# Kernel tuning notes

Hardware: AMD Instinct MI355X
Metric: run time of the kernel (lower is better)

## Reference

```python
import jax, jax.numpy as jnp
import numpy as np

LN_EPS = 1e-5
DIM = 8        # pooled spatial size per axis -> token feature = DIM*DIM = 64
DIM_HEAD = 64


def setup_inputs() -> dict:
    key = jax.random.key(0)
    k1, k2, k3 = jax.random.split(key, 3)
    b, t, c, h, w = 8, 16, 64, 56, 56
    x = jax.random.normal(k1, (b, t, c, h, w), dtype=jnp.float32)
    pos_embedding = jax.random.normal(k2, (b * c, t, DIM * DIM), dtype=jnp.float32)
    # nn.Linear(dim*dim, 2*dim_head, bias=False); stored here as (in, out)
    W_qk = jax.random.normal(k3, (DIM * DIM, 2 * DIM_HEAD), dtype=jnp.float32) * (DIM * DIM) ** -0.5
    gamma = jnp.ones((DIM * DIM,), dtype=jnp.float32)
    beta = jnp.zeros((DIM * DIM,), dtype=jnp.float32)
    return {"x": x, "pos_embedding": pos_embedding, "W_qk": W_qk, "gamma": gamma, "beta": beta}


def reference(x, pos_embedding, W_qk, gamma, beta):
    b, t, c, h, w = x.shape
    scale = DIM_HEAD ** -0.5
    # AdaptiveAvgPool3d((None, DIM, DIM)): h,w divisible by DIM -> exact mean pool
    ph, pw = h // DIM, w // DIM
    pooled = x.reshape(b, t, c, DIM, ph, DIM, pw).mean(axis=(4, 6))  # (b,t,c,DIM,DIM)
    # rearrange 'b t c h w -> (b c) t (h w)'
    s = jnp.transpose(pooled, (0, 2, 1, 3, 4)).reshape(b * c, t, DIM * DIM)
    s = s + pos_embedding
    # LayerNorm over last dim
    mu = s.mean(axis=-1, keepdims=True)
    var = s.var(axis=-1, keepdims=True)
    s = (s - mu) * jax.lax.rsqrt(var + LN_EPS) * gamma + beta
    qk = s @ W_qk                                   # (bc, t, 2*dim_head)
    q, k = jnp.split(qk, 2, axis=-1)
    v = jnp.transpose(x, (0, 2, 1, 3, 4)).reshape(b * c, t, h * w)
    dots = jnp.einsum('bid,bjd->bij', q, k) * scale  # (bc, t, t)
    attn = jax.nn.softmax(dots, axis=-1)             # dropout in eval mode = identity
    out = jnp.einsum('bij,bjf->bif', attn, v)        # (bc, t, h*w)
    out = out.reshape(b, c, t, h, w).transpose(0, 2, 1, 3, 4)
    return out + x
```

## Files before the change

### kernel.cpp

```cpp
#include <hip/hip_runtime.h>
#include <hip/hip_bf16.h>
#include <math.h>


#define HW 3136
#define HW4 784
#define TSTRIDE4 50176

typedef float vfloat4 __attribute__((ext_vector_type(4)));

__global__ __launch_bounds__(256) void pool_kernel(const float* __restrict__ x,
                                                   const float* __restrict__ pos,
                                                   float* __restrict__ s_ws) {
    __shared__ float plane[HW];
    const int p   = blockIdx.x;
    const int tid = threadIdx.x;

    const float4* xp = reinterpret_cast<const float4*>(x + (size_t)p * HW);
    float4* pl4 = reinterpret_cast<float4*>(plane);
    #pragma unroll
    for (int k = 0; k < 3; k++) pl4[tid + k * 256] = xp[tid + k * 256];
    if (tid < 16) pl4[768 + tid] = xp[768 + tid];
    __syncthreads();

    if (tid < 64) {
        const int i = tid >> 3, j = tid & 7;
        const float* base = plane + (i * 7) * 56 + j * 7;
        float sum = 0.f;
        #pragma unroll
        for (int r = 0; r < 7; r++) {
            #pragma unroll
            for (int cc = 0; cc < 7; cc++) sum += base[r * 56 + cc];
        }
        const int c = p & 63, t = (p >> 6) & 15, b = p >> 10;
        const int bc = b * 64 + c;
        const int off = ((bc << 4) + t) * 64 + tid;
        s_ws[off] = sum * (1.0f / 49.0f) + pos[off];
    }
}

__device__ __forceinline__ void acc4(vfloat4& a, float w, const float4& v) {
    a.x += w * v.x; a.y += w * v.y; a.z += w * v.z; a.w += w * v.w;
}

__global__ __launch_bounds__(256) void attn_apply_kernel(const float* __restrict__ x,
                                                         const float* __restrict__ s_ws,
                                                         const float* __restrict__ W,
                                                         const float* __restrict__ gamma,
                                                         const float* __restrict__ beta,
                                                         float* __restrict__ out) {
    __shared__ float s_lds[16 * 64];
    __shared__ float q_lds[16 * 65];
    __shared__ float k_lds[16 * 65];
    __shared__ float A[256];

    const int bc  = blockIdx.x;
    const int qtr = blockIdx.y;
    const int tid = threadIdx.x;

    const float4* S4 = reinterpret_cast<const float4*>(s_ws + (size_t)bc * 1024);
    reinterpret_cast<float4*>(s_lds)[tid] = S4[tid];
    __syncthreads();

    {
        const int row = tid >> 4, sub = tid & 15;
        float4 v = *reinterpret_cast<const float4*>(&s_lds[row * 64 + sub * 4]);
        float sum = v.x + v.y + v.z + v.w;
        float sq  = v.x * v.x + v.y * v.y + v.z * v.z + v.w * v.w;
        #pragma unroll
        for (int off = 8; off > 0; off >>= 1) {
            sum += __shfl_xor(sum, off, 64);
            sq  += __shfl_xor(sq,  off, 64);
        }
        const float mu  = sum * (1.0f / 64.0f);
        const float var = sq * (1.0f / 64.0f) - mu * mu;
        const float rs  = rsqrtf(var + 1e-5f);
        const float4 g  = *reinterpret_cast<const float4*>(&gamma[sub * 4]);
        const float4 bt = *reinterpret_cast<const float4*>(&beta[sub * 4]);
        float4 o;
        o.x = (v.x - mu) * rs * g.x + bt.x;
        o.y = (v.y - mu) * rs * g.y + bt.y;
        o.z = (v.z - mu) * rs * g.z + bt.z;
        o.w = (v.w - mu) * rs * g.w + bt.w;
        *reinterpret_cast<float4*>(&s_lds[row * 64 + sub * 4]) = o;
    }
    __syncthreads();

    {
        const int col = tid & 127;
        const int rb  = (tid >> 7) * 8;
        float wcol[64];
        #pragma unroll
        for (int d = 0; d < 64; d++) wcol[d] = W[d * 128 + col];
        float qa[8];
        #pragma unroll
        for (int r = 0; r < 8; r++) {
            float a = 0.f;
            #pragma unroll
            for (int dd = 0; dd < 16; dd++) {
                const float4 sv = *reinterpret_cast<const float4*>(&s_lds[(rb + r) * 64 + dd * 4]);
                a += sv.x * wcol[dd * 4 + 0] + sv.y * wcol[dd * 4 + 1]
                   + sv.z * wcol[dd * 4 + 2] + sv.w * wcol[dd * 4 + 3];
            }
            qa[r] = a;
        }
        if (col < 64) {
            #pragma unroll
            for (int r = 0; r < 8; r++) q_lds[(rb + r) * 65 + col] = qa[r];
        } else {
            #pragma unroll
            for (int r = 0; r < 8; r++) k_lds[(rb + r) * 65 + (col - 64)] = qa[r];
        }
    }
    __syncthreads();

    {
        const int i = tid >> 4, j = tid & 15;
        float dot = 0.f;
        #pragma unroll
        for (int d = 0; d < 64; d++)
            dot += q_lds[i * 65 + d] * k_lds[j * 65 + d];
        dot *= 0.125f;
        float m = dot;
        #pragma unroll
        for (int off = 8; off > 0; off >>= 1)
            m = fmaxf(m, __shfl_xor(m, off, 64));
        const float e = __expf(dot - m);
        float es = e;
        #pragma unroll
        for (int off = 8; off > 0; off >>= 1)
            es += __shfl_xor(es, off, 64);
        A[i * 16 + j] = e / es + (i == j ? 1.0f : 0.0f);
    }
    __syncthreads();

    if (tid < 196) {
        const int b = bc >> 6, c = bc & 63;
        const size_t f4i = (size_t)qtr * 196 + tid;
        const float4* x4 = reinterpret_cast<const float4*>(x);
        vfloat4* o4 = reinterpret_cast<vfloat4*>(out);
        const size_t plane0 = ((size_t)b * 1024 + c) * HW4;

        float4 xv[16];
        #pragma unroll
        for (int j = 0; j < 16; j++)
            xv[j] = x4[plane0 + (size_t)j * TSTRIDE4 + f4i];

        #pragma unroll
        for (int t = 0; t < 16; t++) {
            vfloat4 a = (vfloat4)(0.f);
            #pragma unroll
            for (int jj = 0; jj < 4; jj++) {
                const float4 w4 = *reinterpret_cast<const float4*>(&A[t * 16 + jj * 4]);
                acc4(a, w4.x, xv[jj * 4 + 0]);
                acc4(a, w4.y, xv[jj * 4 + 1]);
                acc4(a, w4.z, xv[jj * 4 + 2]);
                acc4(a, w4.w, xv[jj * 4 + 3]);
            }
            __builtin_nontemporal_store(a, &o4[plane0 + (size_t)t * TSTRIDE4 + f4i]);
        }
    }
}

extern "C" void kernel_launch(void* const* d_in, const int* in_sizes, int n_in,
                              void* d_out, int out_size, void* d_ws, size_t ws_size,
                              hipStream_t stream) {
    (void)in_sizes; (void)n_in; (void)out_size; (void)ws_size;
    const float* x     = (const float*)d_in[0];
    const float* pos   = (const float*)d_in[1];
    const float* W     = (const float*)d_in[2];
    const float* gamma = (const float*)d_in[3];
    const float* beta  = (const float*)d_in[4];
    float* out = (float*)d_out;

    float* s_ws = (float*)d_ws;

    pool_kernel<<<8192, 256, 0, stream>>>(x, pos, s_ws);
    attn_apply_kernel<<<dim3(512, 4), 256, 0, stream>>>(x, s_ws, W, gamma, beta, out);
}
```

Baseline: 62.70 us.

## Fuse pooling and attention into one kernel reading x once into registers

Merges the pooling kernel into the attention/apply kernel. Each 1024-thread block loads its whole (b,c) slab of x into registers once, pools it plane by plane through double-buffered LDS, and reuses the same registers for the attention-weighted output. This removes the second full read of x and the workspace round trip. W is also staged in LDS for the projection. The risks are heavy register and LDS use, which limit occupancy, and a serialized pooling loop with many barriers.

```diff
diff --git a/kernel.cpp b/kernel.cpp
--- a/kernel.cpp
+++ b/kernel.cpp
@@ -9,100 +9,96 @@
 
 typedef float vfloat4 __attribute__((ext_vector_type(4)));
 
-__global__ __launch_bounds__(256) void pool_kernel(const float* __restrict__ x,
-                                                   const float* __restrict__ pos,
-                                                   float* __restrict__ s_ws) {
-    __shared__ float plane[HW];
-    const int p   = blockIdx.x;
-    const int tid = threadIdx.x;
-
-    const float4* xp = reinterpret_cast<const float4*>(x + (size_t)p * HW);
-    float4* pl4 = reinterpret_cast<float4*>(plane);
-    #pragma unroll
-    for (int k = 0; k < 3; k++) pl4[tid + k * 256] = xp[tid + k * 256];
-    if (tid < 16) pl4[768 + tid] = xp[768 + tid];
-    __syncthreads();
-
-    if (tid < 64) {
-        const int i = tid >> 3, j = tid & 7;
-        const float* base = plane + (i * 7) * 56 + j * 7;
-        float sum = 0.f;
-        #pragma unroll
-        for (int r = 0; r < 7; r++) {
-            #pragma unroll
-            for (int cc = 0; cc < 7; cc++) sum += base[r * 56 + cc];
-        }
-        const int c = p & 63, t = (p >> 6) & 15, b = p >> 10;
-        const int bc = b * 64 + c;
-        const int off = ((bc << 4) + t) * 64 + tid;
-        s_ws[off] = sum * (1.0f / 49.0f) + pos[off];
-    }
-}
-
 __device__ __forceinline__ void acc4(vfloat4& a, float w, const float4& v) {
     a.x += w * v.x; a.y += w * v.y; a.z += w * v.z; a.w += w * v.w;
 }
 
-__global__ __launch_bounds__(256) void attn_apply_kernel(const float* __restrict__ x,
-                                                         const float* __restrict__ s_ws,
-                                                         const float* __restrict__ W,
-                                                         const float* __restrict__ gamma,
-                                                         const float* __restrict__ beta,
-                                                         float* __restrict__ out) {
+__global__ __launch_bounds__(1024) void fused_kernel(const float* __restrict__ x,
+                                                     const float* __restrict__ pos,
+                                                     const float* __restrict__ W,
+                                                     const float* __restrict__ gamma,
+                                                     const float* __restrict__ beta,
+                                                     float* __restrict__ out) {
+    __shared__ float planebuf[2][HW];
+    __shared__ float w_lds[64 * 128];
     __shared__ float s_lds[16 * 64];
     __shared__ float q_lds[16 * 65];
     __shared__ float k_lds[16 * 65];
     __shared__ float A[256];
 
     const int bc  = blockIdx.x;
-    const int qtr = blockIdx.y;
     const int tid = threadIdx.x;
+    const int b = bc >> 6, c = bc & 63;
+    const size_t plane0 = ((size_t)b * 1024 + c) * HW4;
+    const float4* x4 = reinterpret_cast<const float4*>(x);
 
-    const float4* S4 = reinterpret_cast<const float4*>(s_ws + (size_t)bc * 1024);
-    reinterpret_cast<float4*>(s_lds)[tid] = S4[tid];
+    float4 xv[16];
+    if (tid < 784) {
+        #pragma unroll
+        for (int t = 0; t < 16; t++)
+            xv[t] = x4[plane0 + (size_t)t * TSTRIDE4 + tid];
+    }
+    const float posv = pos[(size_t)bc * 1024 + tid];
+    const float gv = gamma[tid & 63];
+    const float bv = beta[tid & 63];
+
+    {
+        const float4* W4 = reinterpret_cast<const float4*>(W);
+        float4* wl4 = reinterpret_cast<float4*>(w_lds);
+        wl4[tid]        = W4[tid];
+        wl4[tid + 1024] = W4[tid + 1024];
+    }
+
+    if (tid < 784)
+        reinterpret_cast<float4*>(planebuf[0])[tid] = xv[0];
+    #pragma unroll
+    for (int t = 0; t < 16; t++) {
+        __syncthreads();
+        if (t < 15 && tid < 784)
+            reinterpret_cast<float4*>(planebuf[(t + 1) & 1])[tid] = xv[t + 1];
+        if (tid < 64) {
+            const int i = tid >> 3, j = tid & 7;
+            const float* base = planebuf[t & 1] + (i * 7) * 56 + j * 7;
+            float sum = 0.f;
+            #pragma unroll
+            for (int r = 0; r < 7; r++) {
+                #pragma unroll
+                for (int cc = 0; cc < 7; cc++) sum += base[r * 56 + cc];
+            }
+            s_lds[t * 64 + tid] = sum;
+        }
+    }
     __syncthreads();
 
     {
-        const int row = tid >> 4, sub = tid & 15;
-        float4 v = *reinterpret_cast<const float4*>(&s_lds[row * 64 + sub * 4]);
-        float sum = v.x + v.y + v.z + v.w;
-        float sq  = v.x * v.x + v.y * v.y + v.z * v.z + v.w * v.w;
+        float v = s_lds[tid] * (1.0f / 49.0f) + posv;
+        float sum = v, sq = v * v;
         #pragma unroll
-        for (int off = 8; off > 0; off >>= 1) {
+        for (int off = 32; off > 0; off >>= 1) {
             sum += __shfl_xor(sum, off, 64);
             sq  += __shfl_xor(sq,  off, 64);
         }
         const float mu  = sum * (1.0f / 64.0f);
         const float var = sq * (1.0f / 64.0f) - mu * mu;
-        const float rs  = rsqrtf(var + 1e-5f);
-        const float4 g  = *reinterpret_cast<const float4*>(&gamma[sub * 4]);
-        const float4 bt = *reinterpret_cast<const float4*>(&beta[sub * 4]);
-        float4 o;
-        o.x = (v.x - mu) * rs * g.x + bt.x;
-        o.y = (v.y - mu) * rs * g.y + bt.y;
-        o.z = (v.z - mu) * rs * g.z + bt.z;
-        o.w = (v.w - mu) * rs * g.w + bt.w;
-        *reinterpret_cast<float4*>(&s_lds[row * 64 + sub * 4]) = o;
+        s_lds[tid] = (v - mu) * rsqrtf(var + 1e-5f) * gv + bv;
     }
     __syncthreads();
 
-    {
+    if (tid < 256) {
         const int col = tid & 127;
         const int rb  = (tid >> 7) * 8;
-        float wcol[64];
+        float qa[8] = {0.f, 0.f, 0.f, 0.f, 0.f, 0.f, 0.f, 0.f};
         #pragma unroll
-        for (int d = 0; d < 64; d++) wcol[d] = W[d * 128 + col];
-        float qa[8];
-        #pragma unroll
-        for (int r = 0; r < 8; r++) {
-            float a = 0.f;
+        for (int dd = 0; dd < 16; dd++) {
+            const float w0 = w_lds[(dd * 4 + 0) * 128 + col];
+            const float w1 = w_lds[(dd * 4 + 1) * 128 + col];
+            const float w2 = w_lds[(dd * 4 + 2) * 128 + col];
+            const float w3 = w_lds[(dd * 4 + 3) * 128 + col];
             #pragma unroll
-            for (int dd = 0; dd < 16; dd++) {
-                const float4 sv = *reinterpret_cast<const float4*>(&s_lds[(rb + r) * 64 + dd * 4]);
-                a += sv.x * wcol[dd * 4 + 0] + sv.y * wcol[dd * 4 + 1]
-                   + sv.z * wcol[dd * 4 + 2] + sv.w * wcol[dd * 4 + 3];
+            for (int r = 0; r < 8; r++) {
+                const float4 s4 = *reinterpret_cast<const float4*>(&s_lds[(rb + r) * 64 + dd * 4]);
+                qa[r] += s4.x * w0 + s4.y * w1 + s4.z * w2 + s4.w * w3;
             }
-            qa[r] = a;
         }
         if (col < 64) {
             #pragma unroll
@@ -114,7 +110,7 @@
     }
     __syncthreads();
 
-    {
+    if (tid < 256) {
         const int i = tid >> 4, j = tid & 15;
         float dot = 0.f;
         #pragma unroll
@@ -134,18 +130,8 @@
     }
     __syncthreads();
 
-    if (tid < 196) {
-        const int b = bc >> 6, c = bc & 63;
-        const size_t f4i = (size_t)qtr * 196 + tid;
-        const float4* x4 = reinterpret_cast<const float4*>(x);
+    if (tid < 784) {
         vfloat4* o4 = reinterpret_cast<vfloat4*>(out);
-        const size_t plane0 = ((size_t)b * 1024 + c) * HW4;
-
-        float4 xv[16];
-        #pragma unroll
-        for (int j = 0; j < 16; j++)
-            xv[j] = x4[plane0 + (size_t)j * TSTRIDE4 + f4i];
-
         #pragma unroll
         for (int t = 0; t < 16; t++) {
             vfloat4 a = (vfloat4)(0.f);
@@ -157,7 +143,7 @@
                 acc4(a, w4.z, xv[jj * 4 + 2]);
                 acc4(a, w4.w, xv[jj * 4 + 3]);
             }
-            __builtin_nontemporal_store(a, &o4[plane0 + (size_t)t * TSTRIDE4 + f4i]);
+            __builtin_nontemporal_store(a, &o4[plane0 + (size_t)t * TSTRIDE4 + tid]);
         }
     }
 }
@@ -165,7 +151,7 @@
 extern "C" void kernel_launch(void* const* d_in, const int* in_sizes, int n_in,
                               void* d_out, int out_size, void* d_ws, size_t ws_size,
                               hipStream_t stream) {
-    (void)in_sizes; (void)n_in; (void)out_size; (void)ws_size;
+    (void)in_sizes; (void)n_in; (void)out_size; (void)d_ws; (void)ws_size;
     const float* x     = (const float*)d_in[0];
     const float* pos   = (const float*)d_in[1];
     const float* W     = (const float*)d_in[2];
@@ -173,8 +159,5 @@
     const float* beta  = (const float*)d_in[4];
     float* out = (float*)d_out;
 
-    float* s_ws = (float*)d_ws;
-
-    pool_kernel<<<8192, 256, 0, stream>>>(x, pos, s_ws);
-    attn_apply_kernel<<<dim3(512, 4), 256, 0, stream>>>(x, s_ws, W, gamma, beta, out);
+    fused_kernel<<<512, 1024, 0, stream>>>(x, pos, W, gamma, beta, out);
 }
```

After: 70.90 us. 13.1% more time.
